# Performance work log

Measured on AMD Instinct MI355X. Metric: run time of the kernel, lower is better.

## Reference

```python
import jax, jax.numpy as jnp
import numpy as np
import math

HIDDEN = 1024
HEADS = 16
HEAD_DIM = HIDDEN // HEADS
LN_EPS = 1e-5


def setup_inputs() -> dict:
    key = jax.random.key(0)
    ks = jax.random.split(key, 11)
    B, S, D = 4, 2048, HIDDEN
    s = 1.0 / math.sqrt(D)
    inp = {
        "x": jax.random.normal(ks[0], (B, S, D), dtype=jnp.float32),
        "mask": jnp.ones((B, S), dtype=jnp.int32),
        "Wq": jax.random.normal(ks[1], (D, D), dtype=jnp.float32) * s,
        "bq": jnp.zeros((D,), dtype=jnp.float32),
        "Wk": jax.random.normal(ks[2], (D, D), dtype=jnp.float32) * s,
        "bk": jnp.zeros((D,), dtype=jnp.float32),
        "Wv": jax.random.normal(ks[3], (D, D), dtype=jnp.float32) * s,
        "bv": jnp.zeros((D,), dtype=jnp.float32),
        "Wo": jax.random.normal(ks[4], (D, D), dtype=jnp.float32) * s,
        "bo": jnp.zeros((D,), dtype=jnp.float32),
        "gamma": jnp.ones((D,), dtype=jnp.float32),
        "beta": jnp.zeros((D,), dtype=jnp.float32),
    }
    return inp


def reference(x, mask, Wq, bq, Wk, bk, Wv, bv, Wo, bo, gamma, beta):
    B, S, D = x.shape
    H, Hd = HEADS, HEAD_DIM
    # torch Linear: y = x @ W.T + b
    def proj(W, b):
        return (x @ W.T + b).reshape(B, S, H, Hd).transpose(0, 2, 1, 3)  # [B,H,S,Hd]
    Q = proj(Wq, bq)
    K = proj(Wk, bk)
    V = proj(Wv, bv)
    scores = jnp.einsum("bhqd,bhkd->bhqk", Q, K) / math.sqrt(Hd)
    # mask [B,S] -> [B,1,1,S]; masked_fill where mask == 0
    m = mask[:, None, None, :]
    scores = jnp.where(m == 0, jnp.float32(-1e9), scores)
    attn = jax.nn.softmax(scores, axis=-1)  # dropout is identity in eval
    context = jnp.einsum("bhqk,bhkd->bhqd", attn, V)
    context = context.transpose(0, 2, 1, 3).reshape(B, S, D)
    out = context @ Wo.T + bo
    y = x + out
    mu = jnp.mean(y, axis=-1, keepdims=True)
    var = jnp.mean(jnp.square(y - mu), axis=-1, keepdims=True)
    return (y - mu) / jnp.sqrt(var + LN_EPS) * gamma + beta
```

## Files before the change

kernel.cpp:

```cpp
#include <hip/hip_runtime.h>

#define D_  1024
#define S_  2048
#define B_  4
#define H_  16
#define HD_ 64
#define BS_ (B_*S_)

#define BM 128
#define BN 128
#define BK 32
#define NT (D_ / BK)

typedef __attribute__((ext_vector_type(8))) short short8;
typedef __attribute__((ext_vector_type(4))) float floatx4;
typedef __attribute__((ext_vector_type(4))) unsigned int uint4v;

typedef __attribute__((address_space(3))) unsigned int lds_uint;
typedef const __attribute__((address_space(1))) unsigned int glob_uint;

#define WS_XB ((size_t)0)
#define WS_WQ ((size_t)16 << 20)
#define WS_WK ((size_t)18 << 20)
#define WS_WV ((size_t)20 << 20)
#define WS_WO ((size_t)22 << 20)
#define WS_Q  ((size_t)24 << 20)
#define WS_KK ((size_t)40 << 20)
#define WS_VT ((size_t)56 << 20)
#define WS_Y  WS_Q

static __device__ __forceinline__ unsigned short f2bf(float f) {
  unsigned u = __builtin_bit_cast(unsigned, f);
  unsigned r = (u + 0x7fffu + ((u >> 16) & 1u)) >> 16;
  return (unsigned short)r;
}

static __device__ __forceinline__ unsigned cvtpk_bf16(float lo, float hi) {
  unsigned r;
  asm("v_cvt_pk_bf16_f32 %0, %1, %2" : "=v"(r) : "v"(lo), "v"(hi));
  return r;
}

static __device__ __forceinline__ float exp2_fast(float x) {
  float r;
  asm("v_exp_f32 %0, %1" : "=v"(r) : "v"(x));
  return r;
}

#define PSWAP(a, b) asm("v_permlane32_swap_b32 %0, %1" : "+v"(a), "+v"(b))

__global__ __launch_bounds__(256) void cvt_f32_bf16(
    const float* __restrict__ src, unsigned short* __restrict__ dst, int n4)
{
  int i = blockIdx.x * 256 + threadIdx.x;
  if (i < n4) {
    float4 v = ((const float4*)src)[i];
    ushort4 o;
    o.x = f2bf(v.x); o.y = f2bf(v.y); o.z = f2bf(v.z); o.w = f2bf(v.w);
    ((ushort4*)dst)[i] = o;
  }
}

#define GEMM_MAINLOOP(Aptr, Bptr)                                              \
  __shared__ unsigned short lds[2][2][BM * BK];                                \
  const int tid  = threadIdx.x;                                                \
  const int wv   = tid >> 6;                                                   \
  const int lane = tid & 63;                                                   \
  const int c    = lane & 15;                                                  \
  const int quad = lane >> 4;                                                  \
  const int srow = lane >> 2;                                                  \
  const int scol = (lane & 3) * 8;                                             \
  const unsigned short* gA = (Aptr) + (size_t)(m0 + wv * 16 + srow) * D_ + scol;\
  const unsigned short* gB = (Bptr) + (size_t)(n0 + wv * 16 + srow) * D_ + scol;\
  const int lbase = (wv * 16) * BK;                                            \
  const int wr = (wv >> 1) * 64;                                               \
  const int wc = (wv & 1) * 64;                                                \
  floatx4 acc[4][4];                                                           \
  _Pragma("unroll")                                                            \
  for (int mi = 0; mi < 4; ++mi)                                               \
    _Pragma("unroll")                                                          \
    for (int ni = 0; ni < 4; ++ni) acc[mi][ni] = (floatx4){0.f,0.f,0.f,0.f};   \
  auto stage = [&](int buf, int t) {                                           \
    const size_t koff = (size_t)t * BK;                                        \
    _Pragma("unroll")                                                          \
    for (int j = 0; j < 2; ++j) {                                              \
      __builtin_amdgcn_global_load_lds(                                        \
          (glob_uint*)(gA + (size_t)j * 64 * D_ + koff),                       \
          (lds_uint*)&lds[buf][0][j * 64 * BK + lbase], 16, 0, 0);             \
      __builtin_amdgcn_global_load_lds(                                        \
          (glob_uint*)(gB + (size_t)j * 64 * D_ + koff),                       \
          (lds_uint*)&lds[buf][1][j * 64 * BK + lbase], 16, 0, 0);             \
    }                                                                          \
  };                                                                           \
  stage(0, 0);                                                                 \
  __syncthreads();                                                             \
  int cur = 0;                                                                 \
  for (int t = 0; t < NT; ++t) {                                               \
    if (t + 1 < NT) stage(cur ^ 1, t + 1);                                     \
    const unsigned short* LA = &lds[cur][0][0];                                \
    const unsigned short* LB = &lds[cur][1][0];                                \
    short8 af[4], bf[4];                                                       \
    _Pragma("unroll")                                                          \
    for (int i = 0; i < 4; ++i) {                                              \
      af[i] = *(const short8*)&LA[(wr + i * 16 + c) * BK + quad * 8];          \
      bf[i] = *(const short8*)&LB[(wc + i * 16 + c) * BK + quad * 8];          \
    }                                                                          \
    _Pragma("unroll")                                                          \
    for (int mi = 0; mi < 4; ++mi)                                             \
      _Pragma("unroll")                                                        \
      for (int ni = 0; ni < 4; ++ni)                                           \
        acc[mi][ni] = __builtin_amdgcn_mfma_f32_16x16x32_bf16(                 \
            af[mi], bf[ni], acc[mi][ni], 0, 0, 0);                             \
    __syncthreads();                                                           \
    cur ^= 1;                                                                  \
  }

__global__ __launch_bounds__(256) void gemm_qkv(
    const unsigned short* __restrict__ X,
    const unsigned short* __restrict__ Wq, const float* __restrict__ bq,
    const unsigned short* __restrict__ Wk, const float* __restrict__ bk,
    const unsigned short* __restrict__ Wv, const float* __restrict__ bv,
    unsigned short* __restrict__ Qo, unsigned short* __restrict__ Ko,
    unsigned short* __restrict__ Vo)
{
  const int i    = blockIdx.x;
  const int o    = (i & 7) * (1536 / 8) + (i >> 3);
  const int mode = o % 3;
  const int r    = o / 3;
  const int m0   = (r >> 3) * BM;
  const int n0   = (r & 7) * BN;

  const unsigned short* W = (mode == 0) ? Wq : ((mode == 1) ? Wk : Wv);
  const float* bias       = (mode == 0) ? bq : ((mode == 1) ? bk : bv);
  unsigned short* dst     = (mode == 0) ? Qo : ((mode == 1) ? Ko : Vo);

  GEMM_MAINLOOP(X, W)

  const int b = m0 >> 11;
  #pragma unroll
  for (int mi = 0; mi < 4; ++mi) {
    const int sb = (m0 & (S_ - 1)) + wr + mi * 16 + quad * 4;
    #pragma unroll
    for (int ni = 0; ni < 4; ++ni) {
      const int n   = n0 + wc + ni * 16 + c;
      const float bv_ = bias[n];
      const int h  = n >> 6;
      const int hd = n & 63;
      if (mode < 2) {
        size_t base = ((size_t)((b * H_ + h) * S_ + sb)) * HD_ + hd;
        #pragma unroll
        for (int r2 = 0; r2 < 4; ++r2)
          dst[base + (size_t)r2 * HD_] = f2bf(acc[mi][ni][r2] + bv_);
      } else {
        size_t base = ((size_t)((b * H_ + h) * HD_ + hd)) * S_ + sb;
        ushort4 ov;
        ov.x = f2bf(acc[mi][ni][0] + bv_);
        ov.y = f2bf(acc[mi][ni][1] + bv_);
        ov.z = f2bf(acc[mi][ni][2] + bv_);
        ov.w = f2bf(acc[mi][ni][3] + bv_);
        *(ushort4*)&dst[base] = ov;
      }
    }
  }
}

__global__ __launch_bounds__(256)
void attn_kernel(
    const unsigned short* __restrict__ Q, const unsigned short* __restrict__ K,
    const unsigned short* __restrict__ Vt, const int* __restrict__ mask,
    unsigned short* __restrict__ ctx)
{
  __shared__ unsigned short Kl[2][4096];
  __shared__ unsigned short Vl[2][4096];

  const int wv   = threadIdx.x >> 6;
  const int lane = threadIdx.x & 63;
  const int c    = lane & 15;
  const int quad = lane >> 4;

  const int id = blockIdx.x;
  const int bh = (id & 7) + 8 * (id >> 7);
  const int qt = (id >> 3) & 15;
  const int b  = bh >> 4;
  const int h  = bh & 15;
  const int q0 = qt * 128 + wv * 32;

  const unsigned short* Qb = Q  + (size_t)bh * S_ * HD_;
  const unsigned short* Kb = K  + (size_t)bh * S_ * HD_;
  const unsigned short* Vb = Vt + (size_t)bh * HD_ * S_;
  const int* mrow = mask + b * S_;

  short8 bQ[2][2];
  #pragma unroll
  for (int s = 0; s < 2; ++s) {
    const unsigned short* qrow = Qb + (size_t)(q0 + s * 16 + c) * HD_;
    bQ[s][0] = *(const short8*)(qrow + quad * 8);
    bQ[s][1] = *(const short8*)(qrow + 32 + quad * 8);
  }

  short8 ones;
  #pragma unroll
  for (int i = 0; i < 8; ++i) ones[i] = (short)0x3F80;

  floatx4 acc[2][4], accl[2];
  #pragma unroll
  for (int s = 0; s < 2; ++s) {
    #pragma unroll
    for (int d = 0; d < 4; ++d) acc[s][d] = (floatx4){0.f, 0.f, 0.f, 0.f};
    accl[s] = (floatx4){0.f, 0.f, 0.f, 0.f};
  }

  const float SC = 0.125f * 1.44269504089f;

  auto stageKV = [&](int buf, int kp0) {
    #pragma unroll
    for (int j = 0; j < 2; ++j) {
      const int Pb  = j * 256 + (wv << 6);
      const int P   = Pb + lane;
      const int row = P >> 3;
      const int c8  = (P & 7) ^ (row & 7);
      __builtin_amdgcn_global_load_lds(
          (glob_uint*)(Kb + (size_t)(kp0 + row) * HD_ + c8 * 8),
          (lds_uint*)&Kl[buf][Pb * 8], 16, 0, 0);
      __builtin_amdgcn_global_load_lds(
          (glob_uint*)(Vb + (size_t)row * S_ + kp0 + c8 * 8),
          (lds_uint*)&Vl[buf][Pb * 8], 16, 0, 0);
    }
  };

  stageKV(0, 0);
  __syncthreads();
  int cur = 0;

  for (int t = 0; t < S_ / 64; ++t) {
    const int kp0 = t * 64;
    if (t + 1 < S_ / 64) stageKV(cur ^ 1, kp0 + 64);

    int4 mk4[4];
    #pragma unroll
    for (int ct = 0; ct < 4; ++ct)
      mk4[ct] = *(const int4*)(mrow + kp0 + ct * 16 + quad * 4);

    floatx4 Cm[2][4];
    #pragma unroll
    for (int kt2 = 0; kt2 < 4; ++kt2) {
      const int krow = kt2 * 16 + c;
      const int sw   = krow & 7;
      short8 k0 = *(const short8*)&Kl[cur][krow * 64 + ((quad) ^ sw) * 8];
      short8 k1 = *(const short8*)&Kl[cur][krow * 64 + ((4 + quad) ^ sw) * 8];
      floatx4 z0 = {0.f,0.f,0.f,0.f}, z1 = {0.f,0.f,0.f,0.f};
      z0 = __builtin_amdgcn_mfma_f32_16x16x32_bf16(k0, bQ[0][0], z0, 0, 0, 0);
      z1 = __builtin_amdgcn_mfma_f32_16x16x32_bf16(k0, bQ[1][0], z1, 0, 0, 0);
      z0 = __builtin_amdgcn_mfma_f32_16x16x32_bf16(k1, bQ[0][1], z0, 0, 0, 0);
      z1 = __builtin_amdgcn_mfma_f32_16x16x32_bf16(k1, bQ[1][1], z1, 0, 0, 0);
      Cm[0][kt2] = z0;
      Cm[1][kt2] = z1;
    }

    unsigned w[2][4][2];
    #pragma unroll
    for (int ct = 0; ct < 4; ++ct) {
      const float mb0 = (mk4[ct].x == 0) ? -1e30f : 0.f;
      const float mb1 = (mk4[ct].y == 0) ? -1e30f : 0.f;
      const float mb2 = (mk4[ct].z == 0) ? -1e30f : 0.f;
      const float mb3 = (mk4[ct].w == 0) ? -1e30f : 0.f;
      #pragma unroll
      for (int s = 0; s < 2; ++s) {
        float p0 = exp2_fast(fmaf(Cm[s][ct][0], SC, mb0));
        float p1 = exp2_fast(fmaf(Cm[s][ct][1], SC, mb1));
        float p2 = exp2_fast(fmaf(Cm[s][ct][2], SC, mb2));
        float p3 = exp2_fast(fmaf(Cm[s][ct][3], SC, mb3));
        w[s][ct][0] = cvtpk_bf16(p0, p1);
        w[s][ct][1] = cvtpk_bf16(p2, p3);
      }
    }

    #pragma unroll
    for (int ch = 0; ch < 2; ++ch) {
      short8 pf[2];
      #pragma unroll
      for (int s = 0; s < 2; ++s) {
        unsigned a0 = w[s][2 * ch][0],     a1 = w[s][2 * ch][1];
        unsigned b0 = w[s][2 * ch + 1][0], b1 = w[s][2 * ch + 1][1];
        PSWAP(a0, b0);
        PSWAP(a1, b1);
        uint4v pw = {a0, a1, b0, b1};
        pf[s] = __builtin_bit_cast(short8, pw);
      }
      const int c0 = ch * 4 + (quad >> 1) * 2;
      const int h0 = (quad & 1) * 4;
      #pragma unroll
      for (int dt = 0; dt < 4; ++dt) {
        const int vrow = dt * 16 + c;
        const int sw   = vrow & 7;
        uint2 vlo = *(const uint2*)&Vl[cur][vrow * 64 + ((c0)     ^ sw) * 8 + h0];
        uint2 vhi = *(const uint2*)&Vl[cur][vrow * 64 + ((c0 + 1) ^ sw) * 8 + h0];
        uint4v vw = {vlo.x, vlo.y, vhi.x, vhi.y};
        short8 vf = __builtin_bit_cast(short8, vw);
        acc[0][dt] = __builtin_amdgcn_mfma_f32_16x16x32_bf16(vf, pf[0], acc[0][dt], 0, 0, 0);
        acc[1][dt] = __builtin_amdgcn_mfma_f32_16x16x32_bf16(vf, pf[1], acc[1][dt], 0, 0, 0);
      }
      accl[0] = __builtin_amdgcn_mfma_f32_16x16x32_bf16(ones, pf[0], accl[0], 0, 0, 0);
      accl[1] = __builtin_amdgcn_mfma_f32_16x16x32_bf16(ones, pf[1], accl[1], 0, 0, 0);
    }

    __syncthreads();
    cur ^= 1;
  }

  #pragma unroll
  for (int s = 0; s < 2; ++s) {
    const float inv = 1.f / accl[s][0];
    #pragma unroll
    for (int dt = 0; dt < 4; ++dt) {
      ushort4 o;
      o.x = f2bf(acc[s][dt][0] * inv);
      o.y = f2bf(acc[s][dt][1] * inv);
      o.z = f2bf(acc[s][dt][2] * inv);
      o.w = f2bf(acc[s][dt][3] * inv);
      *(ushort4*)&ctx[((size_t)(b * S_ + q0 + s * 16 + c)) * D_ +
                      h * HD_ + dt * 16 + quad * 4] = o;
    }
  }
}

__global__ __launch_bounds__(256) void gemm_out(
    const unsigned short* __restrict__ CTX, const unsigned short* __restrict__ W,
    const float* __restrict__ bo, const float* __restrict__ X,
    float* __restrict__ Y)
{
  const int i  = blockIdx.x;
  const int o  = (i & 7) * (512 / 8) + (i >> 3);
  const int m0 = (o >> 3) * BM;
  const int n0 = (o & 7) * BN;

  GEMM_MAINLOOP(CTX, W)

  #pragma unroll
  for (int mi = 0; mi < 4; ++mi) {
    const int m = m0 + wr + mi * 16 + quad * 4;
    #pragma unroll
    for (int ni = 0; ni < 4; ++ni) {
      const int n = n0 + wc + ni * 16 + c;
      const float bias = bo[n];
      #pragma unroll
      for (int r2 = 0; r2 < 4; ++r2)
        Y[(size_t)(m + r2) * D_ + n] =
            acc[mi][ni][r2] + bias + X[(size_t)(m + r2) * D_ + n];
    }
  }
}

__global__ __launch_bounds__(256) void ln_kernel(
    const float* __restrict__ Y, const float* __restrict__ gamma,
    const float* __restrict__ beta, float* __restrict__ out)
{
  __shared__ float red[2][4];
  const int row  = blockIdx.x;
  const int tid  = threadIdx.x;
  const int wv   = tid >> 6;
  const int lane = tid & 63;
  const float* y = Y + (size_t)row * D_;

  float v[4];
  float sum = 0.f, sumsq = 0.f;
  #pragma unroll
  for (int i = 0; i < 4; ++i) {
    v[i] = y[tid + i * 256];
    sum += v[i];
    sumsq += v[i] * v[i];
  }
  #pragma unroll
  for (int off = 32; off > 0; off >>= 1) {
    sum   += __shfl_down(sum, off, 64);
    sumsq += __shfl_down(sumsq, off, 64);
  }
  if (lane == 0) { red[0][wv] = sum; red[1][wv] = sumsq; }
  __syncthreads();
  sum   = red[0][0] + red[0][1] + red[0][2] + red[0][3];
  sumsq = red[1][0] + red[1][1] + red[1][2] + red[1][3];

  const float mu   = sum * (1.f / D_);
  const float var  = sumsq * (1.f / D_) - mu * mu;
  const float rstd = rsqrtf(var + 1e-5f);

  #pragma unroll
  for (int i = 0; i < 4; ++i) {
    const int col = tid + i * 256;
    out[(size_t)row * D_ + col] = (v[i] - mu) * rstd * gamma[col] + beta[col];
  }
}

extern "C" void kernel_launch(void* const* d_in, const int* in_sizes, int n_in,
                              void* d_out, int out_size, void* d_ws, size_t ws_size,
                              hipStream_t stream) {
  const float* x     = (const float*)d_in[0];
  const int*   mask  = (const int*)d_in[1];
  const float* Wq    = (const float*)d_in[2];
  const float* bq    = (const float*)d_in[3];
  const float* Wk    = (const float*)d_in[4];
  const float* bk    = (const float*)d_in[5];
  const float* Wv    = (const float*)d_in[6];
  const float* bv    = (const float*)d_in[7];
  const float* Wo    = (const float*)d_in[8];
  const float* bo    = (const float*)d_in[9];
  const float* gamma = (const float*)d_in[10];
  const float* beta  = (const float*)d_in[11];

  char* ws = (char*)d_ws;
  unsigned short* xb    = (unsigned short*)(ws + WS_XB);
  unsigned short* wqb   = (unsigned short*)(ws + WS_WQ);
  unsigned short* wkb   = (unsigned short*)(ws + WS_WK);
  unsigned short* wvb   = (unsigned short*)(ws + WS_WV);
  unsigned short* wob   = (unsigned short*)(ws + WS_WO);
  unsigned short* q_ws  = (unsigned short*)(ws + WS_Q);
  unsigned short* k_ws  = (unsigned short*)(ws + WS_KK);
  unsigned short* vt_ws = (unsigned short*)(ws + WS_VT);
  float*          y_ws  = (float*)(ws + WS_Y);
  unsigned short* ctx   = (unsigned short*)d_out;

  const int nx4 = (BS_ * D_) / 4;
  const int nw4 = (D_ * D_) / 4;
  cvt_f32_bf16<<<(nx4 + 255) / 256, 256, 0, stream>>>(x,  xb,  nx4);
  cvt_f32_bf16<<<(nw4 + 255) / 256, 256, 0, stream>>>(Wq, wqb, nw4);
  cvt_f32_bf16<<<(nw4 + 255) / 256, 256, 0, stream>>>(Wk, wkb, nw4);
  cvt_f32_bf16<<<(nw4 + 255) / 256, 256, 0, stream>>>(Wv, wvb, nw4);
  cvt_f32_bf16<<<(nw4 + 255) / 256, 256, 0, stream>>>(Wo, wob, nw4);

  gemm_qkv<<<dim3(1536), 256, 0, stream>>>(
      xb, wqb, bq, wkb, bk, wvb, bv, q_ws, k_ws, vt_ws);

  attn_kernel<<<dim3(16 * 64), 256, 0, stream>>>(
      q_ws, k_ws, vt_ws, mask, ctx);

  gemm_out<<<dim3(512), 256, 0, stream>>>(
      ctx, wob, bo, x, y_ws);

  ln_kernel<<<BS_, 256, 0, stream>>>(y_ws, gamma, beta, (float*)d_out);
}
```

Baseline: 331.3 us.

## Merge conversion launches, load V directly to registers, fuse softmax, vectorize LayerNorm

Replaces the five fp32-to-bf16 conversion launches with a single kernel that picks source and destination by index range. In attention, V tiles are now read straight from global memory into registers instead of staged through LDS, and the exp/convert step is folded into the QK^T MFMA loop. LayerNorm switches to float4 loads and stores. The V change removes LDS traffic and LDS footprint but exposes the attention loop to global-memory latency for V, since those loads are no longer double-buffered.

```diff
diff --git a/kernel.cpp b/kernel.cpp
--- a/kernel.cpp
+++ b/kernel.cpp
@@ -49,16 +49,32 @@
 
 #define PSWAP(a, b) asm("v_permlane32_swap_b32 %0, %1" : "+v"(a), "+v"(b))
 
-__global__ __launch_bounds__(256) void cvt_f32_bf16(
-    const float* __restrict__ src, unsigned short* __restrict__ dst, int n4)
+#define N4_X  ((BS_ * D_) / 4)
+#define N4_W  ((D_ * D_) / 4)
+__global__ __launch_bounds__(256) void cvt_all(
+    const float* __restrict__ x,
+    const float* __restrict__ Wq, const float* __restrict__ Wk,
+    const float* __restrict__ Wv, const float* __restrict__ Wo,
+    unsigned short* __restrict__ xb,
+    unsigned short* __restrict__ wqb, unsigned short* __restrict__ wkb,
+    unsigned short* __restrict__ wvb, unsigned short* __restrict__ wob)
 {
   int i = blockIdx.x * 256 + threadIdx.x;
-  if (i < n4) {
-    float4 v = ((const float4*)src)[i];
-    ushort4 o;
-    o.x = f2bf(v.x); o.y = f2bf(v.y); o.z = f2bf(v.z); o.w = f2bf(v.w);
-    ((ushort4*)dst)[i] = o;
-  }
+  const float* src;
+  unsigned short* dst;
+  if (i < N4_X) {
+    src = x; dst = xb;
+  } else {
+    int j = i - N4_X;
+    int w = j / N4_W;
+    i = j - w * N4_W;
+    src = (w == 0) ? Wq : (w == 1) ? Wk : (w == 2) ? Wv : Wo;
+    dst = (w == 0) ? wqb : (w == 1) ? wkb : (w == 2) ? wvb : wob;
+  }
+  float4 v = ((const float4*)src)[i];
+  ushort4 o;
+  o.x = f2bf(v.x); o.y = f2bf(v.y); o.z = f2bf(v.z); o.w = f2bf(v.w);
+  ((ushort4*)dst)[i] = o;
 }
 
 #define GEMM_MAINLOOP(Aptr, Bptr)                                              \
@@ -171,7 +187,6 @@
     unsigned short* __restrict__ ctx)
 {
   __shared__ unsigned short Kl[2][4096];
-  __shared__ unsigned short Vl[2][4096];
 
   const int wv   = threadIdx.x >> 6;
   const int lane = threadIdx.x & 63;
@@ -211,8 +226,9 @@
   }
 
   const float SC = 0.125f * 1.44269504089f;
-
-  auto stageKV = [&](int buf, int kp0) {
+  const int voff = (quad & 1) * 4 + (quad >> 1) * 16;
+
+  auto stageK = [&](int buf, int kp0) {
     #pragma unroll
     for (int j = 0; j < 2; ++j) {
       const int Pb  = j * 256 + (wv << 6);
@@ -222,26 +238,34 @@
       __builtin_amdgcn_global_load_lds(
           (glob_uint*)(Kb + (size_t)(kp0 + row) * HD_ + c8 * 8),
           (lds_uint*)&Kl[buf][Pb * 8], 16, 0, 0);
-      __builtin_amdgcn_global_load_lds(
-          (glob_uint*)(Vb + (size_t)row * S_ + kp0 + c8 * 8),
-          (lds_uint*)&Vl[buf][Pb * 8], 16, 0, 0);
     }
   };
 
-  stageKV(0, 0);
+  stageK(0, 0);
   __syncthreads();
   int cur = 0;
 
   for (int t = 0; t < S_ / 64; ++t) {
     const int kp0 = t * 64;
-    if (t + 1 < S_ / 64) stageKV(cur ^ 1, kp0 + 64);
+    if (t + 1 < S_ / 64) stageK(cur ^ 1, kp0 + 64);
 
     int4 mk4[4];
     #pragma unroll
     for (int ct = 0; ct < 4; ++ct)
       mk4[ct] = *(const int4*)(mrow + kp0 + ct * 16 + quad * 4);
 
-    floatx4 Cm[2][4];
+    uint2 vl[2][4], vh[2][4];
+    #pragma unroll
+    for (int ch = 0; ch < 2; ++ch)
+      #pragma unroll
+      for (int dt = 0; dt < 4; ++dt) {
+        const unsigned short* vrow =
+            Vb + (size_t)(dt * 16 + c) * S_ + kp0 + ch * 32 + voff;
+        vl[ch][dt] = *(const uint2*)(vrow);
+        vh[ch][dt] = *(const uint2*)(vrow + 8);
+      }
+
+    unsigned w[2][4][2];
     #pragma unroll
     for (int kt2 = 0; kt2 < 4; ++kt2) {
       const int krow = kt2 * 16 + c;
@@ -253,25 +277,26 @@
       z1 = __builtin_amdgcn_mfma_f32_16x16x32_bf16(k0, bQ[1][0], z1, 0, 0, 0);
       z0 = __builtin_amdgcn_mfma_f32_16x16x32_bf16(k1, bQ[0][1], z0, 0, 0, 0);
       z1 = __builtin_amdgcn_mfma_f32_16x16x32_bf16(k1, bQ[1][1], z1, 0, 0, 0);
-      Cm[0][kt2] = z0;
-      Cm[1][kt2] = z1;
-    }
-
-    unsigned w[2][4][2];
-    #pragma unroll
-    for (int ct = 0; ct < 4; ++ct) {
-      const float mb0 = (mk4[ct].x == 0) ? -1e30f : 0.f;
-      const float mb1 = (mk4[ct].y == 0) ? -1e30f : 0.f;
-      const float mb2 = (mk4[ct].z == 0) ? -1e30f : 0.f;
-      const float mb3 = (mk4[ct].w == 0) ? -1e30f : 0.f;
-      #pragma unroll
-      for (int s = 0; s < 2; ++s) {
-        float p0 = exp2_fast(fmaf(Cm[s][ct][0], SC, mb0));
-        float p1 = exp2_fast(fmaf(Cm[s][ct][1], SC, mb1));
-        float p2 = exp2_fast(fmaf(Cm[s][ct][2], SC, mb2));
-        float p3 = exp2_fast(fmaf(Cm[s][ct][3], SC, mb3));
-        w[s][ct][0] = cvtpk_bf16(p0, p1);
-        w[s][ct][1] = cvtpk_bf16(p2, p3);
+
+      const float mb0 = (mk4[kt2].x == 0) ? -1e30f : 0.f;
+      const float mb1 = (mk4[kt2].y == 0) ? -1e30f : 0.f;
+      const float mb2 = (mk4[kt2].z == 0) ? -1e30f : 0.f;
+      const float mb3 = (mk4[kt2].w == 0) ? -1e30f : 0.f;
+      {
+        float p0 = exp2_fast(fmaf(z0[0], SC, mb0));
+        float p1 = exp2_fast(fmaf(z0[1], SC, mb1));
+        float p2 = exp2_fast(fmaf(z0[2], SC, mb2));
+        float p3 = exp2_fast(fmaf(z0[3], SC, mb3));
+        w[0][kt2][0] = cvtpk_bf16(p0, p1);
+        w[0][kt2][1] = cvtpk_bf16(p2, p3);
+      }
+      {
+        float p0 = exp2_fast(fmaf(z1[0], SC, mb0));
+        float p1 = exp2_fast(fmaf(z1[1], SC, mb1));
+        float p2 = exp2_fast(fmaf(z1[2], SC, mb2));
+        float p3 = exp2_fast(fmaf(z1[3], SC, mb3));
+        w[1][kt2][0] = cvtpk_bf16(p0, p1);
+        w[1][kt2][1] = cvtpk_bf16(p2, p3);
       }
     }
 
@@ -287,15 +312,9 @@
         uint4v pw = {a0, a1, b0, b1};
         pf[s] = __builtin_bit_cast(short8, pw);
       }
-      const int c0 = ch * 4 + (quad >> 1) * 2;
-      const int h0 = (quad & 1) * 4;
       #pragma unroll
       for (int dt = 0; dt < 4; ++dt) {
-        const int vrow = dt * 16 + c;
-        const int sw   = vrow & 7;
-        uint2 vlo = *(const uint2*)&Vl[cur][vrow * 64 + ((c0)     ^ sw) * 8 + h0];
-        uint2 vhi = *(const uint2*)&Vl[cur][vrow * 64 + ((c0 + 1) ^ sw) * 8 + h0];
-        uint4v vw = {vlo.x, vlo.y, vhi.x, vhi.y};
+        uint4v vw = {vl[ch][dt].x, vl[ch][dt].y, vh[ch][dt].x, vh[ch][dt].y};
         short8 vf = __builtin_bit_cast(short8, vw);
         acc[0][dt] = __builtin_amdgcn_mfma_f32_16x16x32_bf16(vf, pf[0], acc[0][dt], 0, 0, 0);
         acc[1][dt] = __builtin_amdgcn_mfma_f32_16x16x32_bf16(vf, pf[1], acc[1][dt], 0, 0, 0);
@@ -362,14 +381,10 @@
   const int lane = tid & 63;
   const float* y = Y + (size_t)row * D_;
 
-  float v[4];
-  float sum = 0.f, sumsq = 0.f;
-  #pragma unroll
-  for (int i = 0; i < 4; ++i) {
-    v[i] = y[tid + i * 256];
-    sum += v[i];
-    sumsq += v[i] * v[i];
-  }
+  float4 v = ((const float4*)y)[tid];
+  float sum   = (v.x + v.y) + (v.z + v.w);
+  float sumsq = (v.x * v.x + v.y * v.y) + (v.z * v.z + v.w * v.w);
+
   #pragma unroll
   for (int off = 32; off > 0; off >>= 1) {
     sum   += __shfl_down(sum, off, 64);
@@ -384,11 +399,14 @@
   const float var  = sumsq * (1.f / D_) - mu * mu;
   const float rstd = rsqrtf(var + 1e-5f);
 
-  #pragma unroll
-  for (int i = 0; i < 4; ++i) {
-    const int col = tid + i * 256;
-    out[(size_t)row * D_ + col] = (v[i] - mu) * rstd * gamma[col] + beta[col];
-  }
+  const float4 g = ((const float4*)gamma)[tid];
+  const float4 bt = ((const float4*)beta)[tid];
+  float4 o;
+  o.x = (v.x - mu) * rstd * g.x + bt.x;
+  o.y = (v.y - mu) * rstd * g.y + bt.y;
+  o.z = (v.z - mu) * rstd * g.z + bt.z;
+  o.w = (v.w - mu) * rstd * g.w + bt.w;
+  ((float4*)(out + (size_t)row * D_))[tid] = o;
 }
 
 extern "C" void kernel_launch(void* const* d_in, const int* in_sizes, int n_in,
@@ -419,13 +437,9 @@
   float*          y_ws  = (float*)(ws + WS_Y);
   unsigned short* ctx   = (unsigned short*)d_out;
 
-  const int nx4 = (BS_ * D_) / 4;
-  const int nw4 = (D_ * D_) / 4;
-  cvt_f32_bf16<<<(nx4 + 255) / 256, 256, 0, stream>>>(x,  xb,  nx4);
-  cvt_f32_bf16<<<(nw4 + 255) / 256, 256, 0, stream>>>(Wq, wqb, nw4);
-  cvt_f32_bf16<<<(nw4 + 255) / 256, 256, 0, stream>>>(Wk, wkb, nw4);
-  cvt_f32_bf16<<<(nw4 + 255) / 256, 256, 0, stream>>>(Wv, wvb, nw4);
-  cvt_f32_bf16<<<(nw4 + 255) / 256, 256, 0, stream>>>(Wo, wob, nw4);
+  const int n4_total = N4_X + 4 * N4_W;
+  cvt_all<<<(n4_total + 255) / 256, 256, 0, stream>>>(
+      x, Wq, Wk, Wv, Wo, xb, wqb, wkb, wvb, wob);
 
   gemm_qkv<<<dim3(1536), 256, 0, stream>>>(
       xb, wqb, bq, wkb, bk, wvb, bv, q_ws, k_ws, vt_ws);
```

Result: slower. 469.2 us (+41.6%).

## Merge conversion launches, enlarge attention blocks, vectorize LayerNorm

Applied to the files above, without the earlier changes.

Combines the five fp32-to-bf16 conversion launches into one kernel that dispatches on the global index. Doubles the attention block to 512 threads covering 256 queries, so each staged K/V tile is shared by eight waves and K/V staging traffic per query drops. Vectorizes LayerNorm loads and stores with float4. The larger attention blocks reduce the block count and may cut occupancy or balance across CUs.

```diff
diff --git a/kernel.cpp b/kernel.cpp
--- a/kernel.cpp
+++ b/kernel.cpp
@@ -49,16 +49,32 @@
 
 #define PSWAP(a, b) asm("v_permlane32_swap_b32 %0, %1" : "+v"(a), "+v"(b))
 
-__global__ __launch_bounds__(256) void cvt_f32_bf16(
-    const float* __restrict__ src, unsigned short* __restrict__ dst, int n4)
+#define N4_X  ((BS_ * D_) / 4)
+#define N4_W  ((D_ * D_) / 4)
+__global__ __launch_bounds__(256) void cvt_all(
+    const float* __restrict__ x,
+    const float* __restrict__ Wq, const float* __restrict__ Wk,
+    const float* __restrict__ Wv, const float* __restrict__ Wo,
+    unsigned short* __restrict__ xb,
+    unsigned short* __restrict__ wqb, unsigned short* __restrict__ wkb,
+    unsigned short* __restrict__ wvb, unsigned short* __restrict__ wob)
 {
   int i = blockIdx.x * 256 + threadIdx.x;
-  if (i < n4) {
-    float4 v = ((const float4*)src)[i];
-    ushort4 o;
-    o.x = f2bf(v.x); o.y = f2bf(v.y); o.z = f2bf(v.z); o.w = f2bf(v.w);
-    ((ushort4*)dst)[i] = o;
-  }
+  const float* src;
+  unsigned short* dst;
+  if (i < N4_X) {
+    src = x; dst = xb;
+  } else {
+    int j = i - N4_X;
+    int w = j / N4_W;
+    i = j - w * N4_W;
+    src = (w == 0) ? Wq : (w == 1) ? Wk : (w == 2) ? Wv : Wo;
+    dst = (w == 0) ? wqb : (w == 1) ? wkb : (w == 2) ? wvb : wob;
+  }
+  float4 v = ((const float4*)src)[i];
+  ushort4 o;
+  o.x = f2bf(v.x); o.y = f2bf(v.y); o.z = f2bf(v.z); o.w = f2bf(v.w);
+  ((ushort4*)dst)[i] = o;
 }
 
 #define GEMM_MAINLOOP(Aptr, Bptr)                                              \
@@ -164,7 +180,7 @@
   }
 }
 
-__global__ __launch_bounds__(256)
+__global__ __launch_bounds__(512)
 void attn_kernel(
     const unsigned short* __restrict__ Q, const unsigned short* __restrict__ K,
     const unsigned short* __restrict__ Vt, const int* __restrict__ mask,
@@ -179,11 +195,11 @@
   const int quad = lane >> 4;
 
   const int id = blockIdx.x;
-  const int bh = (id & 7) + 8 * (id >> 7);
-  const int qt = (id >> 3) & 15;
+  const int bh = (id & 7) + 8 * (id >> 6);
+  const int qt = (id >> 3) & 7;
   const int b  = bh >> 4;
   const int h  = bh & 15;
-  const int q0 = qt * 128 + wv * 32;
+  const int q0 = qt * 256 + wv * 32;
 
   const unsigned short* Qb = Q  + (size_t)bh * S_ * HD_;
   const unsigned short* Kb = K  + (size_t)bh * S_ * HD_;
@@ -213,19 +229,16 @@
   const float SC = 0.125f * 1.44269504089f;
 
   auto stageKV = [&](int buf, int kp0) {
-    #pragma unroll
-    for (int j = 0; j < 2; ++j) {
-      const int Pb  = j * 256 + (wv << 6);
-      const int P   = Pb + lane;
-      const int row = P >> 3;
-      const int c8  = (P & 7) ^ (row & 7);
-      __builtin_amdgcn_global_load_lds(
-          (glob_uint*)(Kb + (size_t)(kp0 + row) * HD_ + c8 * 8),
-          (lds_uint*)&Kl[buf][Pb * 8], 16, 0, 0);
-      __builtin_amdgcn_global_load_lds(
-          (glob_uint*)(Vb + (size_t)row * S_ + kp0 + c8 * 8),
-          (lds_uint*)&Vl[buf][Pb * 8], 16, 0, 0);
-    }
+    const int Pb  = wv << 6;
+    const int P   = Pb + lane;
+    const int row = P >> 3;
+    const int c8  = (P & 7) ^ (row & 7);
+    __builtin_amdgcn_global_load_lds(
+        (glob_uint*)(Kb + (size_t)(kp0 + row) * HD_ + c8 * 8),
+        (lds_uint*)&Kl[buf][Pb * 8], 16, 0, 0);
+    __builtin_amdgcn_global_load_lds(
+        (glob_uint*)(Vb + (size_t)row * S_ + kp0 + c8 * 8),
+        (lds_uint*)&Vl[buf][Pb * 8], 16, 0, 0);
   };
 
   stageKV(0, 0);
@@ -362,14 +375,10 @@
   const int lane = tid & 63;
   const float* y = Y + (size_t)row * D_;
 
-  float v[4];
-  float sum = 0.f, sumsq = 0.f;
-  #pragma unroll
-  for (int i = 0; i < 4; ++i) {
-    v[i] = y[tid + i * 256];
-    sum += v[i];
-    sumsq += v[i] * v[i];
-  }
+  float4 v = ((const float4*)y)[tid];
+  float sum   = (v.x + v.y) + (v.z + v.w);
+  float sumsq = (v.x * v.x + v.y * v.y) + (v.z * v.z + v.w * v.w);
+
   #pragma unroll
   for (int off = 32; off > 0; off >>= 1) {
     sum   += __shfl_down(sum, off, 64);
@@ -384,11 +393,14 @@
   const float var  = sumsq * (1.f / D_) - mu * mu;
   const float rstd = rsqrtf(var + 1e-5f);
 
-  #pragma unroll
-  for (int i = 0; i < 4; ++i) {
-    const int col = tid + i * 256;
-    out[(size_t)row * D_ + col] = (v[i] - mu) * rstd * gamma[col] + beta[col];
-  }
+  const float4 g = ((const float4*)gamma)[tid];
+  const float4 bt = ((const float4*)beta)[tid];
+  float4 o;
+  o.x = (v.x - mu) * rstd * g.x + bt.x;
+  o.y = (v.y - mu) * rstd * g.y + bt.y;
+  o.z = (v.z - mu) * rstd * g.z + bt.z;
+  o.w = (v.w - mu) * rstd * g.w + bt.w;
+  ((float4*)(out + (size_t)row * D_))[tid] = o;
 }
 
 extern "C" void kernel_launch(void* const* d_in, const int* in_sizes, int n_in,
@@ -419,18 +431,14 @@
   float*          y_ws  = (float*)(ws + WS_Y);
   unsigned short* ctx   = (unsigned short*)d_out;
 
-  const int nx4 = (BS_ * D_) / 4;
-  const int nw4 = (D_ * D_) / 4;
-  cvt_f32_bf16<<<(nx4 + 255) / 256, 256, 0, stream>>>(x,  xb,  nx4);
-  cvt_f32_bf16<<<(nw4 + 255) / 256, 256, 0, stream>>>(Wq, wqb, nw4);
-  cvt_f32_bf16<<<(nw4 + 255) / 256, 256, 0, stream>>>(Wk, wkb, nw4);
-  cvt_f32_bf16<<<(nw4 + 255) / 256, 256, 0, stream>>>(Wv, wvb, nw4);
-  cvt_f32_bf16<<<(nw4 + 255) / 256, 256, 0, stream>>>(Wo, wob, nw4);
+  const int n4_total = N4_X + 4 * N4_W;
+  cvt_all<<<(n4_total + 255) / 256, 256, 0, stream>>>(
+      x, Wq, Wk, Wv, Wo, xb, wqb, wkb, wvb, wob);
 
   gemm_qkv<<<dim3(1536), 256, 0, stream>>>(
       xb, wqb, bq, wkb, bk, wvb, bv, q_ws, k_ws, vt_ws);
 
-  attn_kernel<<<dim3(16 * 64), 256, 0, stream>>>(
+  attn_kernel<<<dim3(512), 512, 0, stream>>>(
       q_ws, k_ws, vt_ws, mask, ctx);
 
   gemm_out<<<dim3(512), 256, 0, stream>>>(
```

Result: slower. 369.6 us (+11.5%).
